# Optimization experiments

Hardware: AMD Instinct MI355X
Metric: run time of the kernel (lower is better)

The kernel has to match this reference:

```python
import jax, jax.numpy as jnp
import numpy as np
import math

# Dimensions (see shape_source)
B, C, NH = 4, 256, 8
VP, VW = 6, 16   # vertical: patches-per-window (outer), windows (inner)
HP, HW = 32, 3   # horizontal: patches-per-window (outer), windows (inner)
NW, P = VW * HW, VP * HP   # 48 windows, 192 patches per window
GRID = 96                   # patch grid is 96x96
SHIFT = (HP // 2, VP // 2)  # (16, 3) = (window_shape[0]//2, window_shape[1]//2)
FF = 4 * C
SCALE = 1.0 / math.sqrt(C)  # source divides by sqrt(embedding_dim), not head_dim


def setup_inputs() -> dict:
    key = jax.random.key(0)
    ks = jax.random.split(key, 17)
    std = 0.02
    n = lambda k, s: (jax.random.normal(k, s, dtype=jnp.float32) * std)
    return {
        "embeddings": jax.random.normal(ks[0], (B, GRID, GRID, C), dtype=jnp.float32),
        "ln1_g": jnp.ones((C,), jnp.float32), "ln1_b": jnp.zeros((C,), jnp.float32),
        "wq": n(ks[1], (C, C)), "bq": jnp.zeros((C,), jnp.float32),
        "wk": n(ks[2], (C, C)), "bk": jnp.zeros((C,), jnp.float32),
        "wv": n(ks[3], (C, C)), "bv": jnp.zeros((C,), jnp.float32),
        "pos_bias": n(ks[4], (NH, P, P)),
        "ln2_g": jnp.ones((C,), jnp.float32), "ln2_b": jnp.zeros((C,), jnp.float32),
        "w1": n(ks[5], (C, FF)), "b1": jnp.zeros((FF,), jnp.float32),
        "w2": n(ks[6], (FF, C)), "b2": jnp.zeros((C,), jnp.float32),
    }


def _ln(x, g, b, eps=1e-5):
    m = jnp.mean(x, axis=-1, keepdims=True)
    v = jnp.mean(jnp.square(x - m), axis=-1, keepdims=True)
    return (x - m) * jax.lax.rsqrt(v + eps) * g + b


def reference(embeddings, ln1_g, ln1_b, wq, bq, wk, bk, wv, bv, pos_bias,
              ln2_g, ln2_b, w1, b1, w2, b2):
    x = jnp.roll(embeddings, SHIFT, axis=(1, 2))
    # part: H=(VP outer, VW inner), W=(HP outer, HW inner) -> [B, NW, P, C]
    p = x.reshape(B, VP, VW, HP, HW, C).transpose(0, 2, 4, 1, 3, 5).reshape(B, NW, P, C)
    y = _ln(p, ln1_g, ln1_b)
    def heads(w, b):
        return (y @ w + b).reshape(B, NW, P, NH, C // NH).transpose(0, 1, 3, 2, 4)
    q, k, v = heads(wq, bq), heads(wk, bk), heads(wv, bv)  # [B, NW, NH, P, Dh]
    logits = jnp.einsum('bwhpd,bwhqd->bwhpq', q, k) * SCALE + pos_bias
    attn = jax.nn.softmax(logits, axis=-1)
    sa = jnp.einsum('bwhpq,bwhqd->bwhpd', attn, v)
    sa = sa.transpose(0, 1, 3, 2, 4).reshape(B, NW, P, C)
    a = p + sa
    h = _ln(a, ln2_g, ln2_b)
    ff = jax.nn.gelu(h @ w1 + b1, approximate=False) @ w2 + b2
    out = a + ff
    # join: inverse of part
    o = out.reshape(B, VW, HW, VP, HP, C).transpose(0, 3, 1, 4, 2, 5).reshape(B, GRID, GRID, C)
    return jnp.roll(o, (-SHIFT[0], -SHIFT[1]), axis=(1, 2))
```

## Files before the change

### kernel.cpp

```cpp
#include <hip/hip_runtime.h>
#include <hip/hip_bf16.h>
#include <cstdint>

using bf16x8 = __attribute__((ext_vector_type(8))) short;
using f32x4  = __attribute__((ext_vector_type(4))) float;
using bf16_t = __hip_bfloat16;

#define DEVI static __device__ __forceinline__

constexpr int kB = 4, kC = 256, kNH = 8, kDh = 32;
constexpr int kVP = 6, kVW = 16, kHP = 32, kHW = 3;
constexpr int kNW = 48, kP = 192, kGRID = 96;
constexpr int kRows = kB * kNW * kP;
constexpr int kFF = 1024;
constexpr float kScale = 0.0625f;

DEVI void row_coords(int row, int& b, int& g1, int& g2) {
  int b_  = row / (kNW * kP);
  int rem = row - b_ * (kNW * kP);
  int w = rem / kP;
  int p = rem - w * kP;
  int vw = w / kHW, hw = w - vw * kHW;
  int vp = p >> 5,  hp = p & 31;
  int r  = vp * kVW + vw;
  int cc = hp * kHW + hw;
  g1 = r + 80;  if (g1 >= kGRID) g1 -= kGRID;
  g2 = cc + 93; if (g2 >= kGRID) g2 -= kGRID;
  b = b_;
}

DEVI float bf2f(short s) {
  union { unsigned u; float f; } c;
  c.u = ((unsigned)(unsigned short)s) << 16;
  return c.f;
}
DEVI short f2bf(float f) {
  bf16_t h = __float2bfloat16(f);
  return *reinterpret_cast<short*>(&h);
}

DEVI void gload16(const void* g, void* l) {
  __builtin_amdgcn_global_load_lds(
      (__attribute__((address_space(1))) void*)(uintptr_t)g,
      (__attribute__((address_space(3))) void*)(uintptr_t)l, 16, 0, 0);
}

__global__ __launch_bounds__(256) void k_wconv(
    const float* __restrict__ wq, const float* __restrict__ wk,
    const float* __restrict__ wv, const float* __restrict__ w1,
    const float* __restrict__ w2, bf16_t* __restrict__ W) {
  const int i = blockIdx.x * 256 + threadIdx.x;
  if (i < 196608) {
    const int n = i >> 8, k = i & 255;
    const float* src = n < 256 ? wq : (n < 512 ? wk : wv);
    W[i] = __float2bfloat16(src[k * 256 + (n & 255)]);
  } else if (i < 458752) {
    const int j = i - 196608;
    const int n = j >> 8, k = j & 255;
    W[i] = __float2bfloat16(w1[k * 1024 + n]);
  } else if (i < 720896) {
    const int j = i - 458752;
    const int n = j >> 10, k = j & 1023;
    W[i] = __float2bfloat16(w2[k * 256 + n]);
  }
}

__global__ __launch_bounds__(256) void k_ln1(const float* __restrict__ emb,
    const float* __restrict__ gam, const float* __restrict__ bet,
    bf16_t* __restrict__ Y) {
  const int wave = threadIdx.x >> 6, lane = threadIdx.x & 63;
  #pragma unroll
  for (int rr = 0; rr < 2; ++rr) {
    const int row = blockIdx.x * 8 + wave * 2 + rr;
    int b, g1, g2; row_coords(row, b, g1, g2);
    const float* src = emb + (((size_t)b * kGRID + g1) * kGRID + g2) * kC;
    float4 x = *reinterpret_cast<const float4*>(src + lane * 4);
    float s  = x.x + x.y + x.z + x.w;
    float sq = x.x*x.x + x.y*x.y + x.z*x.z + x.w*x.w;
    #pragma unroll
    for (int off = 32; off; off >>= 1) { s += __shfl_xor(s, off); sq += __shfl_xor(sq, off); }
    const float mean = s * (1.f / kC);
    const float rstd = rsqrtf(sq * (1.f / kC) - mean * mean + 1e-5f);
    const float4 g4 = *reinterpret_cast<const float4*>(gam + lane * 4);
    const float4 b4 = *reinterpret_cast<const float4*>(bet + lane * 4);
    short4 o;
    o.x = f2bf((x.x - mean) * rstd * g4.x + b4.x);
    o.y = f2bf((x.y - mean) * rstd * g4.y + b4.y);
    o.z = f2bf((x.z - mean) * rstd * g4.z + b4.z);
    o.w = f2bf((x.w - mean) * rstd * g4.w + b4.w);
    *reinterpret_cast<short4*>(Y + (size_t)row * kC + lane * 4) = o;
  }
}

__global__ __launch_bounds__(256) void k_ln2(const float* __restrict__ emb,
    const bf16_t* __restrict__ SA,
    const float* __restrict__ gam, const float* __restrict__ bet,
    float* __restrict__ A, bf16_t* __restrict__ H) {
  const int wave = threadIdx.x >> 6, lane = threadIdx.x & 63;
  #pragma unroll
  for (int rr = 0; rr < 2; ++rr) {
    const int row = blockIdx.x * 8 + wave * 2 + rr;
    int b, g1, g2; row_coords(row, b, g1, g2);
    const float* src = emb + (((size_t)b * kGRID + g1) * kGRID + g2) * kC;
    float4 x = *reinterpret_cast<const float4*>(src + lane * 4);
    short4 sv = *reinterpret_cast<const short4*>(SA + (size_t)row * kC + lane * 4);
    x.x += bf2f(sv.x); x.y += bf2f(sv.y); x.z += bf2f(sv.z); x.w += bf2f(sv.w);
    *reinterpret_cast<float4*>(A + (size_t)row * kC + lane * 4) = x;
    float s  = x.x + x.y + x.z + x.w;
    float sq = x.x*x.x + x.y*x.y + x.z*x.z + x.w*x.w;
    #pragma unroll
    for (int off = 32; off; off >>= 1) { s += __shfl_xor(s, off); sq += __shfl_xor(sq, off); }
    const float mean = s * (1.f / kC);
    const float rstd = rsqrtf(sq * (1.f / kC) - mean * mean + 1e-5f);
    const float4 g4 = *reinterpret_cast<const float4*>(gam + lane * 4);
    const float4 b4 = *reinterpret_cast<const float4*>(bet + lane * 4);
    short4 o;
    o.x = f2bf((x.x - mean) * rstd * g4.x + b4.x);
    o.y = f2bf((x.y - mean) * rstd * g4.y + b4.y);
    o.z = f2bf((x.z - mean) * rstd * g4.z + b4.z);
    o.w = f2bf((x.w - mean) * rstd * g4.w + b4.w);
    *reinterpret_cast<short4*>(H + (size_t)row * kC + lane * 4) = o;
  }
}

template <int KDIM, int EPI, int GX>
__global__ __launch_bounds__(256, 2) void k_gemm3(
    const bf16_t* __restrict__ Amat, const bf16_t* __restrict__ BT,
    const float* __restrict__ bias0, const float* __restrict__ bias1,
    const float* __restrict__ bias2,
    bf16_t* __restrict__ Obf, const float* __restrict__ Ares,
    float* __restrict__ Out) {
  __shared__ bf16_t As[2][128 * 64];
  __shared__ bf16_t Bs[2][128 * 64];
  const int tid = threadIdx.x;
  const int wave = tid >> 6, lane = tid & 63;
  const int lr = lane & 15, kgf = lane >> 4;
  const int nwg = (kRows / 128) * GX;
  const int wg = (blockIdx.x & 7) * (nwg >> 3) + (blockIdx.x >> 3);
  const int m0 = (wg / GX) * 128, n0 = (wg % GX) * 128;
  const int wm = (wave >> 1) * 64, wn = (wave & 1) * 64;
  const int srow = lane >> 3;
  const int scol = ((lane & 7) ^ srow) << 3;

  auto stage = [&](bf16_t* aDst, bf16_t* bDst, int k0) {
    #pragma unroll
    for (int i = 0; i < 4; ++i) {
      const int c = wave * 4 + i;
      const int row = c * 8 + srow;
      gload16(Amat + (size_t)(m0 + row) * KDIM + k0 + scol, aDst + c * 512);
      gload16(BT   + (size_t)(n0 + row) * KDIM + k0 + scol, bDst + c * 512);
    }
  };

  f32x4 acc[4][4] = {};
  auto compute = [&](const bf16_t* aSrc, const bf16_t* bSrc) {
    #pragma unroll
    for (int kk = 0; kk < 2; ++kk) {
      const int kgg = kk * 4 + kgf;
      bf16x8 af[4], bq[4];
      #pragma unroll
      for (int m = 0; m < 4; ++m) {
        const int r = wm + m * 16 + lr;
        af[m] = *reinterpret_cast<const bf16x8*>(aSrc + r * 64 + ((kgg ^ (r & 7)) << 3));
      }
      #pragma unroll
      for (int n = 0; n < 4; ++n) {
        const int r = wn + n * 16 + lr;
        bq[n] = *reinterpret_cast<const bf16x8*>(bSrc + r * 64 + ((kgg ^ (r & 7)) << 3));
      }
      #pragma unroll
      for (int m = 0; m < 4; ++m)
        #pragma unroll
        for (int n = 0; n < 4; ++n)
          acc[m][n] = __builtin_amdgcn_mfma_f32_16x16x32_bf16(af[m], bq[n], acc[m][n], 0, 0, 0);
    }
  };

  stage(As[0], Bs[0], 0);
  __syncthreads();
  constexpr int NT = KDIM / 64;
  #pragma unroll
  for (int t = 0; t < NT; ++t) {
    if (t + 1 < NT) stage(As[(t + 1) & 1], Bs[(t + 1) & 1], (t + 1) * 64);
    compute(As[t & 1], Bs[t & 1]);
    __syncthreads();
  }

  #pragma unroll
  for (int m = 0; m < 4; ++m) {
    #pragma unroll
    for (int n = 0; n < 4; ++n) {
      #pragma unroll
      for (int r = 0; r < 4; ++r) {
        const int row = m0 + wm + m * 16 + kgf * 4 + r;
        const int col = n0 + wn + n * 16 + lr;
        float v = acc[m][n][r];
        if constexpr (EPI == 0) {
          const int which = col >> 8, c = col & 255;
          const float* bp = which == 0 ? bias0 : (which == 1 ? bias1 : bias2);
          v += bp[c];
          Obf[(size_t)which * kRows * kC + (size_t)row * kC + c] = __float2bfloat16(v);
        } else if constexpr (EPI == 1) {
          v += bias0[col];
          const float gl = 0.5f * v * (1.f + erff(v * 0.70710678118654752f));
          Obf[(size_t)row * kFF + col] = __float2bfloat16(gl);
        } else {
          v += bias0[col] + Ares[(size_t)row * kC + col];
          int b, g1, g2; row_coords(row, b, g1, g2);
          Out[(((size_t)b * kGRID + g1) * kGRID + g2) * kC + col] = v;
        }
      }
    }
  }
}

constexpr int kKsPad = 40;
constexpr int kVtPad = 200;
constexpr int kPlPad = 200;
__global__ __launch_bounds__(256) void k_attn(
    const bf16_t* __restrict__ Q, const bf16_t* __restrict__ K,
    const bf16_t* __restrict__ V, const float* __restrict__ pos,
    bf16_t* __restrict__ SA) {
  __shared__ short Ks[kP * kKsPad];
  __shared__ short Vt[kDh * kVtPad];
  __shared__ short Pl[4 * 16 * kPlPad];
  const int bw = blockIdx.x >> 3, h = blockIdx.x & 7;
  const int rowbase = bw * kP, colbase = h * kDh;
  const int tid = threadIdx.x, wave = tid >> 6, lane = tid & 63;
  const int lr = lane & 15, kg = lane >> 4;
  const int wq0 = wave * 48;
  const float* pb = pos + (size_t)h * kP * kP;

  #pragma unroll
  for (int i = 0; i < 3; ++i) {
    const int c = tid + i * 256;
    const int row = c >> 2, dch = (c & 3) * 8;
    const size_t gbase = (size_t)(rowbase + row) * kC + colbase + dch;
    bf16x8 kv = *reinterpret_cast<const bf16x8*>(K + gbase);
    *reinterpret_cast<bf16x8*>(&Ks[row * kKsPad + dch]) = kv;
    bf16x8 vv = *reinterpret_cast<const bf16x8*>(V + gbase);
    #pragma unroll
    for (int e = 0; e < 8; ++e) Vt[(dch + e) * kVtPad + row] = vv[e];
  }
  __syncthreads();

  for (int m = 0; m < 3; ++m) {
    const int rbase = wq0 + m * 16;
    bf16x8 aq = *reinterpret_cast<const bf16x8*>(
        Q + (size_t)(rowbase + rbase + lr) * kC + colbase + kg * 8);
    f32x4 s[12];
    #pragma unroll
    for (int n = 0; n < 12; ++n) {
      bf16x8 bk = *reinterpret_cast<const bf16x8*>(&Ks[(n * 16 + lr) * kKsPad + kg * 8]);
      s[n] = __builtin_amdgcn_mfma_f32_16x16x32_bf16(aq, bk, (f32x4){0.f, 0.f, 0.f, 0.f}, 0, 0, 0);
    }
    float mx[4] = {-1e30f, -1e30f, -1e30f, -1e30f};
    #pragma unroll
    for (int n = 0; n < 12; ++n) {
      #pragma unroll
      for (int r = 0; r < 4; ++r) {
        const float lg = fmaf(s[n][r], kScale,
                              pb[(size_t)(rbase + kg * 4 + r) * kP + n * 16 + lr]);
        s[n][r] = lg;
        mx[r] = fmaxf(mx[r], lg);
      }
    }
    #pragma unroll
    for (int r = 0; r < 4; ++r)
      #pragma unroll
      for (int off = 8; off; off >>= 1) mx[r] = fmaxf(mx[r], __shfl_xor(mx[r], off));
    float sm[4] = {0.f, 0.f, 0.f, 0.f};
    #pragma unroll
    for (int n = 0; n < 12; ++n)
      #pragma unroll
      for (int r = 0; r < 4; ++r) {
        const float e = __expf(s[n][r] - mx[r]);
        s[n][r] = e;
        sm[r] += e;
      }
    #pragma unroll
    for (int r = 0; r < 4; ++r) {
      #pragma unroll
      for (int off = 8; off; off >>= 1) sm[r] += __shfl_xor(sm[r], off);
      sm[r] = 1.f / sm[r];
    }
    #pragma unroll
    for (int n = 0; n < 12; ++n)
      #pragma unroll
      for (int r = 0; r < 4; ++r)
        Pl[(wave * 16 + kg * 4 + r) * kPlPad + n * 16 + lr] = f2bf(s[n][r] * sm[r]);
    f32x4 o0 = {0.f, 0.f, 0.f, 0.f}, o1 = {0.f, 0.f, 0.f, 0.f};
    #pragma unroll
    for (int kk = 0; kk < 6; ++kk) {
      bf16x8 ap = *reinterpret_cast<const bf16x8*>(&Pl[(wave * 16 + lr) * kPlPad + kk * 32 + kg * 8]);
      bf16x8 b0 = *reinterpret_cast<const bf16x8*>(&Vt[lr * kVtPad + kk * 32 + kg * 8]);
      bf16x8 b1 = *reinterpret_cast<const bf16x8*>(&Vt[(16 + lr) * kVtPad + kk * 32 + kg * 8]);
      o0 = __builtin_amdgcn_mfma_f32_16x16x32_bf16(ap, b0, o0, 0, 0, 0);
      o1 = __builtin_amdgcn_mfma_f32_16x16x32_bf16(ap, b1, o1, 0, 0, 0);
    }
    bf16_t* sp = SA + (size_t)(rowbase + rbase + kg * 4) * kC + colbase;
    #pragma unroll
    for (int r = 0; r < 4; ++r) {
      sp[(size_t)r * kC + lr]      = __float2bfloat16(o0[r]);
      sp[(size_t)r * kC + 16 + lr] = __float2bfloat16(o1[r]);
    }
  }
}

extern "C" void kernel_launch(void* const* d_in, const int* in_sizes, int n_in,
                              void* d_out, int out_size, void* d_ws, size_t ws_size,
                              hipStream_t stream) {
  const float* emb  = (const float*)d_in[0];
  const float* ln1g = (const float*)d_in[1];
  const float* ln1b = (const float*)d_in[2];
  const float* wq   = (const float*)d_in[3];
  const float* bq   = (const float*)d_in[4];
  const float* wk   = (const float*)d_in[5];
  const float* bk   = (const float*)d_in[6];
  const float* wv   = (const float*)d_in[7];
  const float* bv   = (const float*)d_in[8];
  const float* pos  = (const float*)d_in[9];
  const float* ln2g = (const float*)d_in[10];
  const float* ln2b = (const float*)d_in[11];
  const float* w1   = (const float*)d_in[12];
  const float* b1   = (const float*)d_in[13];
  const float* w2   = (const float*)d_in[14];
  const float* b2   = (const float*)d_in[15];

  char* ws = (char*)d_ws;
  const size_t nYb = (size_t)kRows * kC * 2;
  bf16_t* Y    = (bf16_t*)(ws);
  bf16_t* Qb   = (bf16_t*)(ws + nYb);
  bf16_t* SAb  = (bf16_t*)(ws + nYb * 4);
  float*  Abuf = (float*) (ws + nYb * 5);
  bf16_t* H    = (bf16_t*)(ws + nYb * 5 + (size_t)kRows * kC * 4);
  bf16_t* G    = (bf16_t*)(ws);
  bf16_t* W    = (bf16_t*)(ws + nYb * 5 + (size_t)kRows * kC * 4 + nYb);
  bf16_t* WqkvT = W;
  bf16_t* W1T   = W + 768 * 256;
  bf16_t* W2T   = W1T + 1024 * 256;

  k_wconv<<<2816, 256, 0, stream>>>(wq, wk, wv, w1, w2, W);
  k_ln1<<<kRows / 8, 256, 0, stream>>>(emb, ln1g, ln1b, Y);
  k_gemm3<256, 0, 6><<<(kRows / 128) * 6, 256, 0, stream>>>(
      Y, WqkvT, bq, bk, bv, Qb, nullptr, nullptr);
  k_attn<<<kB * kNW * kNH, 256, 0, stream>>>(
      Qb, Qb + (size_t)kRows * kC, Qb + 2 * (size_t)kRows * kC, pos, SAb);
  k_ln2<<<kRows / 8, 256, 0, stream>>>(emb, SAb, ln2g, ln2b, Abuf, H);
  k_gemm3<256, 1, 8><<<(kRows / 128) * 8, 256, 0, stream>>>(
      H, W1T, b1, nullptr, nullptr, G, nullptr, nullptr);
  k_gemm3<1024, 2, 2><<<(kRows / 128) * 2, 256, 0, stream>>>(
      G, W2T, b2, nullptr, nullptr, nullptr, Abuf, (float*)d_out);
}
```

Before: 199.8 us.

## Use 512-thread GEMM with larger tiles, explicit vmcnt waits and MFMA priority

```diff
diff --git a/kernel.cpp b/kernel.cpp
--- a/kernel.cpp
+++ b/kernel.cpp
@@ -43,6 +43,14 @@
   __builtin_amdgcn_global_load_lds(
       (__attribute__((address_space(1))) void*)(uintptr_t)g,
       (__attribute__((address_space(3))) void*)(uintptr_t)l, 16, 0, 0);
+}
+
+template <int N> DEVI void wait_vm() {
+  if constexpr (N == 0)      asm volatile("s_waitcnt vmcnt(0)" ::: "memory");
+  else if constexpr (N == 4) asm volatile("s_waitcnt vmcnt(4)" ::: "memory");
+  else if constexpr (N == 6) asm volatile("s_waitcnt vmcnt(6)" ::: "memory");
+  else if constexpr (N == 8) asm volatile("s_waitcnt vmcnt(8)" ::: "memory");
+  __builtin_amdgcn_sched_barrier(0);
 }
 
 __global__ __launch_bounds__(256) void k_wconv(
@@ -123,73 +131,91 @@
   }
 }
 
-template <int KDIM, int EPI, int GX>
-__global__ __launch_bounds__(256, 2) void k_gemm3(
+template <int KDIM, int EPI, int BM, int BN, int GX>
+__global__ __launch_bounds__(512, (BM == 128) ? 4 : 2) void k_gemm4(
     const bf16_t* __restrict__ Amat, const bf16_t* __restrict__ BT,
     const float* __restrict__ bias0, const float* __restrict__ bias1,
     const float* __restrict__ bias2,
     bf16_t* __restrict__ Obf, const float* __restrict__ Ares,
     float* __restrict__ Out) {
-  __shared__ bf16_t As[2][128 * 64];
-  __shared__ bf16_t Bs[2][128 * 64];
+  constexpr int FM = BM / 32;
+  constexpr int FN = BN / 64;
+  constexpr int CA = BM / 64;
+  constexpr int CB = BN / 64;
+  constexpr int L  = CA + CB;
+  constexpr int NT = KDIM / 64;
+  __shared__ bf16_t As[2][BM * 64];
+  __shared__ bf16_t Bs[2][BN * 64];
   const int tid = threadIdx.x;
   const int wave = tid >> 6, lane = tid & 63;
   const int lr = lane & 15, kgf = lane >> 4;
-  const int nwg = (kRows / 128) * GX;
+  const int nwg = (kRows / BM) * GX;
   const int wg = (blockIdx.x & 7) * (nwg >> 3) + (blockIdx.x >> 3);
-  const int m0 = (wg / GX) * 128, n0 = (wg % GX) * 128;
-  const int wm = (wave >> 1) * 64, wn = (wave & 1) * 64;
+  const int m0 = (wg / GX) * BM, n0 = (wg % GX) * BN;
+  const int wm = (wave >> 2) * (BM / 2), wn = (wave & 3) * (BN / 4);
   const int srow = lane >> 3;
   const int scol = ((lane & 7) ^ srow) << 3;
 
-  auto stage = [&](bf16_t* aDst, bf16_t* bDst, int k0) {
-    #pragma unroll
-    for (int i = 0; i < 4; ++i) {
-      const int c = wave * 4 + i;
-      const int row = c * 8 + srow;
-      gload16(Amat + (size_t)(m0 + row) * KDIM + k0 + scol, aDst + c * 512);
-      gload16(BT   + (size_t)(n0 + row) * KDIM + k0 + scol, bDst + c * 512);
+  auto stage = [&](int sbuf, int k0) {
+    #pragma unroll
+    for (int i = 0; i < CA; ++i) {
+      const int c = wave * CA + i;
+      gload16(Amat + (size_t)(m0 + c * 8 + srow) * KDIM + k0 + scol,
+              &As[sbuf][c * 512]);
+    }
+    #pragma unroll
+    for (int i = 0; i < CB; ++i) {
+      const int c = wave * CB + i;
+      gload16(BT + (size_t)(n0 + c * 8 + srow) * KDIM + k0 + scol,
+              &Bs[sbuf][c * 512]);
     }
   };
 
-  f32x4 acc[4][4] = {};
-  auto compute = [&](const bf16_t* aSrc, const bf16_t* bSrc) {
+  f32x4 acc[FM][FN] = {};
+  auto compute = [&](int cbuf) {
     #pragma unroll
     for (int kk = 0; kk < 2; ++kk) {
       const int kgg = kk * 4 + kgf;
-      bf16x8 af[4], bq[4];
-      #pragma unroll
-      for (int m = 0; m < 4; ++m) {
+      bf16x8 af[FM], bq[FN];
+      #pragma unroll
+      for (int m = 0; m < FM; ++m) {
         const int r = wm + m * 16 + lr;
-        af[m] = *reinterpret_cast<const bf16x8*>(aSrc + r * 64 + ((kgg ^ (r & 7)) << 3));
-      }
-      #pragma unroll
-      for (int n = 0; n < 4; ++n) {
+        af[m] = *reinterpret_cast<const bf16x8*>(&As[cbuf][r * 64 + ((kgg ^ (r & 7)) << 3)]);
+      }
+      #pragma unroll
+      for (int n = 0; n < FN; ++n) {
         const int r = wn + n * 16 + lr;
-        bq[n] = *reinterpret_cast<const bf16x8*>(bSrc + r * 64 + ((kgg ^ (r & 7)) << 3));
-      }
-      #pragma unroll
-      for (int m = 0; m < 4; ++m)
+        bq[n] = *reinterpret_cast<const bf16x8*>(&Bs[cbuf][r * 64 + ((kgg ^ (r & 7)) << 3)]);
+      }
+      __builtin_amdgcn_s_setprio(1);
+      #pragma unroll
+      for (int m = 0; m < FM; ++m)
         #pragma unroll
-        for (int n = 0; n < 4; ++n)
+        for (int n = 0; n < FN; ++n)
           acc[m][n] = __builtin_amdgcn_mfma_f32_16x16x32_bf16(af[m], bq[n], acc[m][n], 0, 0, 0);
+      __builtin_amdgcn_s_setprio(0);
     }
   };
 
-  stage(As[0], Bs[0], 0);
-  __syncthreads();
-  constexpr int NT = KDIM / 64;
+  stage(0, 0);
   #pragma unroll
   for (int t = 0; t < NT; ++t) {
-    if (t + 1 < NT) stage(As[(t + 1) & 1], Bs[(t + 1) & 1], (t + 1) * 64);
-    compute(As[t & 1], Bs[t & 1]);
-    __syncthreads();
-  }
-
-  #pragma unroll
-  for (int m = 0; m < 4; ++m) {
-    #pragma unroll
-    for (int n = 0; n < 4; ++n) {
+    const int buf = t & 1;
+    if (t + 1 < NT) {
+      stage(buf ^ 1, (t + 1) * 64);
+      wait_vm<L>();
+    } else {
+      wait_vm<0>();
+    }
+    __builtin_amdgcn_s_barrier();
+    compute(buf);
+    __builtin_amdgcn_s_barrier();
+  }
+
+  #pragma unroll
+  for (int m = 0; m < FM; ++m) {
+    #pragma unroll
+    for (int n = 0; n < FN; ++n) {
       #pragma unroll
       for (int r = 0; r < 4; ++r) {
         const int row = m0 + wm + m * 16 + kgf * 4 + r;
@@ -342,13 +368,13 @@
 
   k_wconv<<<2816, 256, 0, stream>>>(wq, wk, wv, w1, w2, W);
   k_ln1<<<kRows / 8, 256, 0, stream>>>(emb, ln1g, ln1b, Y);
-  k_gemm3<256, 0, 6><<<(kRows / 128) * 6, 256, 0, stream>>>(
+  k_gemm4<256, 0, 256, 256, 3><<<(kRows / 256) * 3, 512, 0, stream>>>(
       Y, WqkvT, bq, bk, bv, Qb, nullptr, nullptr);
   k_attn<<<kB * kNW * kNH, 256, 0, stream>>>(
       Qb, Qb + (size_t)kRows * kC, Qb + 2 * (size_t)kRows * kC, pos, SAb);
   k_ln2<<<kRows / 8, 256, 0, stream>>>(emb, SAb, ln2g, ln2b, Abuf, H);
-  k_gemm3<256, 1, 8><<<(kRows / 128) * 8, 256, 0, stream>>>(
+  k_gemm4<256, 1, 256, 256, 4><<<(kRows / 256) * 4, 512, 0, stream>>>(
       H, W1T, b1, nullptr, nullptr, G, nullptr, nullptr);
-  k_gemm3<1024, 2, 2><<<(kRows / 128) * 2, 256, 0, stream>>>(
+  k_gemm4<1024, 2, 128, 128, 2><<<(kRows / 128) * 2, 512, 0, stream>>>(
       G, W2T, b2, nullptr, nullptr, nullptr, Abuf, (float*)d_out);
 }
```

New measurement: 218.7 us. 1.09x slower.
